# Performance work log

Hardware: AMD Instinct MI355X
Metric: run time of the kernel (lower is better)

## Reference

```python
import jax, jax.numpy as jnp
import numpy as np

N_NODES = 50000
N_EDGES = 500000
D_IN = 128
D_HID = 128
C = 1.0          # curvature (same for every layer)
MIN_NORM = 1e-15
MAX_TANH_ARG = 15.0
PROJ_EPS = 4e-3  # float32 boundary eps used by hgcn PoincareBall.proj


def _artanh(x):
    x = jnp.clip(x, -1.0 + 1e-7, 1.0 - 1e-7)
    return 0.5 * (jnp.log1p(x) - jnp.log1p(-x))


def _tanh(x):
    return jnp.tanh(jnp.clip(x, -MAX_TANH_ARG, MAX_TANH_ARG))


def _norm(x):
    return jnp.maximum(jnp.linalg.norm(x, axis=-1, keepdims=True), MIN_NORM)


def proj(x, c):
    # clip points to stay strictly inside the Poincare ball
    n = _norm(x)
    maxnorm = (1.0 - PROJ_EPS) / jnp.sqrt(c)
    return jnp.where(n > maxnorm, x / n * maxnorm, x)


def expmap0(u, c):
    sc = jnp.sqrt(c)
    n = _norm(u)
    return _tanh(sc * n) * u / (sc * n)


def logmap0(p, c):
    sc = jnp.sqrt(c)
    n = _norm(p)
    return _artanh(sc * n) * p / (sc * n)


def mobius_add(x, y, c):
    x2 = jnp.sum(x * x, -1, keepdims=True)
    y2 = jnp.sum(y * y, -1, keepdims=True)
    xy = jnp.sum(x * y, -1, keepdims=True)
    num = (1.0 + 2.0 * c * xy + c * y2) * x + (1.0 - c * x2) * y
    den = 1.0 + 2.0 * c * xy + c * c * x2 * y2
    return num / jnp.maximum(den, MIN_NORM)


def mobius_matvec(m, x, c):
    sc = jnp.sqrt(c)
    xn = _norm(x)
    mx = x @ m.T                                   # [N, out]
    mxn = _norm(mx)
    res = _tanh(mxn / xn * _artanh(sc * xn)) * mx / (mxn * sc)
    is_zero = jnp.all(mx == 0.0, axis=-1, keepdims=True)
    return jnp.where(is_zero, jnp.zeros_like(res), res)


def hyp_linear(x, W, b, c):
    h = proj(mobius_matvec(W, x, c), c)
    hyp_bias = proj(expmap0(b[None, :], c), c)     # proj_tan0 is identity on the ball
    return proj(mobius_add(h, hyp_bias, c), c)


def hyp_agg(x, src, dst, edge_weight, c):
    x_tan = logmap0(x, c)                          # [N, d] tangent at origin
    msg = edge_weight[:, None] * x_tan[src]        # [E, d] gather + scale
    agg = jax.ops.segment_sum(msg, dst, num_segments=N_NODES)  # spmm(adj, x_tan)
    return proj(expmap0(agg, c), c)


def hyp_act(x, c_in, c_out):
    xt = jax.nn.relu(logmap0(x, c_in))
    return proj(expmap0(xt, c_out), c_out)


def setup_inputs() -> dict:
    key = jax.random.key(0)
    ks = jax.random.split(key, 8)
    x = jax.random.normal(ks[0], (N_NODES, D_IN), dtype=jnp.float32) * 0.1
    src = jax.random.randint(ks[1], (N_EDGES,), 0, N_NODES)
    dst = jax.random.randint(ks[2], (N_EDGES,), 0, N_NODES)
    edge_weight = jax.random.uniform(ks[3], (N_EDGES,), dtype=jnp.float32) * 0.1
    s1 = 1.0 / np.sqrt(D_IN)
    W1 = jax.random.normal(ks[4], (D_HID, D_IN), dtype=jnp.float32) * s1
    b1 = jax.random.normal(ks[5], (D_HID,), dtype=jnp.float32) * 0.01
    W2 = jax.random.normal(ks[6], (D_HID, D_HID), dtype=jnp.float32) * s1
    b2 = jax.random.normal(ks[7], (D_HID,), dtype=jnp.float32) * 0.01
    return {"x": x, "src": src, "dst": dst, "edge_weight": edge_weight,
            "W1": W1, "b1": b1, "W2": W2, "b2": b2}


def reference(x, src, dst, edge_weight, W1, b1, W2, b2):
    c = jnp.float32(C)
    # HGCN.encode: proj_tan0 (identity for PoincareBall) -> expmap0 -> proj
    h = proj(expmap0(x, c), c)
    # layer 1: HypLinear -> HypAgg -> HypAct
    h = hyp_linear(h, W1, b1, c)
    h = hyp_agg(h, src, dst, edge_weight, c)
    h = hyp_act(h, c, c)
    # layer 2
    h = hyp_linear(h, W2, b2, c)
    h = hyp_agg(h, src, dst, edge_weight, c)
    h = hyp_act(h, c, c)
    return h
```

## Files before the change

### kernel.cpp

```cpp
#include <hip/hip_runtime.h>
#include <math.h>

#define MIN_NORM 1e-15f
#define MAXNORM  0.996f
#define ARTANH_CLIP 0.99999988f

typedef __bf16 bf16x8 __attribute__((ext_vector_type(8)));
typedef float  f32x4  __attribute__((ext_vector_type(4)));

union FragU { ushort u[8]; uint4 q; bf16x8 v; };

__device__ __forceinline__ float wave_sum(float v) {
#pragma unroll
    for (int off = 32; off > 0; off >>= 1) v += __shfl_xor(v, off, 64);
    return v;
}

__device__ __forceinline__ float tanh_fast(float x) {
    const float t = __expf(2.f * fminf(x, 15.f));
    return 1.f - 2.f / (t + 1.f);
}
__device__ __forceinline__ float artanh_fast(float x) {
    x = fminf(x, ARTANH_CLIP);
    return 0.5f * __logf((1.f + x) / (1.f - x));
}

__device__ __forceinline__ float proj_factor(float n2) {
    float n = fmaxf(sqrtf(n2), MIN_NORM);
    return (n > MAXNORM) ? (MAXNORM / n) : 1.f;
}

__device__ __forceinline__ unsigned short f2bf(float f) {
    unsigned u = __float_as_uint(f);
    return (unsigned short)((u + 0x7fffu + ((u >> 16) & 1u)) >> 16);
}
__device__ __forceinline__ float bf2f(unsigned short h) {
    return __uint_as_float((unsigned)h << 16);
}
__device__ __forceinline__ float bflo(unsigned u) { return __uint_as_float(u << 16); }
__device__ __forceinline__ float bfhi(unsigned u) { return __uint_as_float(u & 0xffff0000u); }

__device__ __forceinline__ void red16_f4(float4& v) {
#pragma unroll
    for (int off = 1; off < 16; off <<= 1) {
        v.x += __shfl_xor(v.x, off, 64);
        v.y += __shfl_xor(v.y, off, 64);
        v.z += __shfl_xor(v.z, off, 64);
        v.w += __shfl_xor(v.w, off, 64);
    }
}

__device__ __forceinline__ float bcast_row(const float4& v, int r) {
    const int src = (r >> 2) << 4;
    const float a = __shfl(v.x, src, 64);
    const float b = __shfl(v.y, src, 64);
    const float c = __shfl(v.z, src, 64);
    const float d = __shfl(v.w, src, 64);
    const float lo = (r & 1) ? b : a;
    const float hi = (r & 1) ? d : c;
    return (r & 2) ? hi : lo;
}

__device__ __forceinline__ void pack_w4(const float4 w4, int o, int k, char* out) {
    ushort4 h, l;
    h.x = f2bf(w4.x); l.x = f2bf(w4.x - bf2f(h.x));
    h.y = f2bf(w4.y); l.y = f2bf(w4.y - bf2f(h.y));
    h.z = f2bf(w4.z); l.z = f2bf(w4.z - bf2f(h.z));
    h.w = f2bf(w4.w); l.w = f2bf(w4.w - bf2f(h.w));
    const int prow = ((o & 7) << 4) | (o >> 3);
    const unsigned byte = (unsigned)((prow << 8) + (k << 1)) ^ (unsigned)((prow & 7) << 4);
    *reinterpret_cast<ushort4*>(out + byte) = h;
    *reinterpret_cast<ushort4*>(out + 32768 + byte) = l;
}

__global__ void zero_cnt(int* __restrict__ cnt, int N) {
    const int i = blockIdx.x * blockDim.x + threadIdx.x;
    if (i < N) cnt[i] = 0;
}

__global__ __launch_bounds__(256)
void setup_kernel(const float* __restrict__ W1, const float* __restrict__ W2,
                  char* __restrict__ g1, char* __restrict__ g2,
                  const float* __restrict__ b1, const float* __restrict__ b2,
                  float* __restrict__ hb1, float* __restrict__ hb2,
                  const int* __restrict__ dst, int* __restrict__ cnt, int E) {
    const int b = blockIdx.x;
    if (b < 32) {
        const float* W = (b < 16) ? W1 : W2;
        char* out = (b < 16) ? g1 : g2;
        const int i = (((b & 15) * 256) + threadIdx.x) * 4;
        pack_w4(*reinterpret_cast<const float4*>(&W[i]), i >> 7, i & 127, out);
    } else if (b == 32) {
        if (threadIdx.x < 64) {
            const int lane = threadIdx.x;
#pragma unroll
            for (int j = 0; j < 2; ++j) {
                const float* bb = j ? b2 : b1;
                float* hb = j ? hb2 : hb1;
                float v0 = bb[lane], v1 = bb[lane + 64];
                float n2 = wave_sum(v0 * v0 + v1 * v1);
                float n = fmaxf(sqrtf(n2), MIN_NORM);
                float sc = tanh_fast(n) / n;
                sc *= proj_factor(sc * sc * n2);
                hb[lane] = v0 * sc;
                hb[lane + 64] = v1 * sc;
            }
        }
    } else {
        const int e = (b - 33) * 256 + threadIdx.x;
        if (e < E) atomicAdd(&cnt[dst[e]], 1);
    }
}


__global__ void scan1(const int* __restrict__ cnt, int* __restrict__ ptr,
                      int* __restrict__ bsum, int N) {
    __shared__ int s[256];
    const int t = threadIdx.x;
    const int i = blockIdx.x * 256 + t;
    int v = (i < N) ? ((cnt[i] + 7) & ~7) : 0;
    s[t] = v;
    __syncthreads();
#pragma unroll
    for (int off = 1; off < 256; off <<= 1) {
        int add = (t >= off) ? s[t - off] : 0;
        __syncthreads();
        s[t] += add;
        __syncthreads();
    }
    if (i < N) ptr[i] = s[t] - v;
    if (t == 255) bsum[blockIdx.x] = s[255];
}

__global__ void scan2(const int* __restrict__ bsum, int* __restrict__ bscan, int nb) {
    __shared__ int s[256];
    const int t = threadIdx.x;
    int v = (t < nb) ? bsum[t] : 0;
    s[t] = v;
    __syncthreads();
#pragma unroll
    for (int off = 1; off < 256; off <<= 1) {
        int add = (t >= off) ? s[t - off] : 0;
        __syncthreads();
        s[t] += add;
        __syncthreads();
    }
    bscan[t] = s[t] - v;
    if (t == 255) bscan[256] = s[255];
}

__global__ void scan3(const int* __restrict__ bscan, const int* __restrict__ cnt,
                      int* __restrict__ ptr, int* __restrict__ cursor,
                      unsigned* __restrict__ epk, int N) {
    const int i = blockIdx.x * blockDim.x + threadIdx.x;
    if (i < N) {
        const int p = ptr[i] + bscan[i >> 8];
        ptr[i] = p;
        cursor[i] = p;
        const int c = cnt[i];
        const int pc = (c + 7) & ~7;
        for (int j = c; j < pc; ++j) epk[p + j] = 0u;
    }
    if (i == 0) {
        const int tot = bscan[256];
        ptr[N] = tot;
#pragma unroll
        for (int j = 0; j < 16; ++j) epk[tot + j] = 0u;
    }
}

__global__ void scatter_kernel(const int* __restrict__ src, const int* __restrict__ dst,
                               const float* __restrict__ ew, int* __restrict__ cursor,
                               unsigned* __restrict__ epk, int E) {
    int e = blockIdx.x * blockDim.x + threadIdx.x;
    if (e >= E) return;
    int pos = atomicAdd(&cursor[dst[e]], 1);
    epk[pos] = ((unsigned)src[e] << 16) | (unsigned)f2bf(ew[e]);
}

template <bool PRELUDE, bool BF16IN, bool BF16OUT>
__global__ __launch_bounds__(512, 4)
void hyp_linear_tan_mfma(const void* __restrict__ xin, const char* __restrict__ gWpack,
                         const float* __restrict__ hb, void* __restrict__ xtan,
                         int n_rows) {
    __shared__ __align__(16) char sW[65536];

    const int tid = threadIdx.x;
    const int lane = tid & 63, wid = tid >> 6;
    const int r15 = lane & 15, g = lane >> 4;

    const int tiles = (n_rows + 15) >> 4;
    const int tile = blockIdx.x * 8 + wid;
    const bool active = (tile < tiles);
    const int rowbase = tile << 4;
    const int myrow = rowbase + r15;
    const bool rok = active && (myrow < n_rows);

    float4 xa[4], xb[4];
    uint4 xu[4];
    if (BF16IN) {
        const char* xr = (const char*)xin + (size_t)myrow * 256 + g * 16;
#pragma unroll
        for (int kc = 0; kc < 4; ++kc)
            xu[kc] = rok ? *reinterpret_cast<const uint4*>(xr + kc * 64)
                         : make_uint4(0u, 0u, 0u, 0u);
    } else {
        const float* xr = (const float*)xin + (size_t)myrow * 128 + g * 8;
#pragma unroll
        for (int kc = 0; kc < 4; ++kc) {
            if (rok) {
                xa[kc] = *reinterpret_cast<const float4*>(xr + kc * 32);
                xb[kc] = *reinterpret_cast<const float4*>(xr + kc * 32 + 4);
            } else {
                xa[kc] = make_float4(0.f, 0.f, 0.f, 0.f);
                xb[kc] = xa[kc];
            }
        }
    }

    {
        const uint4* gsrc = reinterpret_cast<const uint4*>(gWpack);
        uint4* ldst = reinterpret_cast<uint4*>(sW);
#pragma unroll
        for (int i = 0; i < 8; ++i) ldst[tid + i * 512] = gsrc[tid + i * 512];
    }

    float yb[8];
    {
        const float4 yba = *reinterpret_cast<const float4*>(&hb[r15 * 8]);
        const float4 ybb = *reinterpret_cast<const float4*>(&hb[r15 * 8 + 4]);
        yb[0] = yba.x; yb[1] = yba.y; yb[2] = yba.z; yb[3] = yba.w;
        yb[4] = ybb.x; yb[5] = ybb.y; yb[6] = ybb.z; yb[7] = ybb.w;
    }
    float y2p = 0.f;
#pragma unroll
    for (int t = 0; t < 8; ++t) y2p += yb[t] * yb[t];
#pragma unroll
    for (int off = 1; off < 16; off <<= 1) y2p += __shfl_xor(y2p, off, 64);
    const float y2 = y2p;

    __syncthreads();
    if (!active) return;

    bf16x8 ah[4], al[4];
    float ss = 0.f;
    if (BF16IN) {
#pragma unroll
        for (int kc = 0; kc < 4; ++kc) {
            FragU fu; fu.q = xu[kc];
            ah[kc] = fu.v;
            const uint4 u = xu[kc];
            float f0 = bflo(u.x), f1 = bfhi(u.x), f2_ = bflo(u.y), f3 = bfhi(u.y);
            float f4 = bflo(u.z), f5 = bfhi(u.z), f6 = bflo(u.w), f7 = bfhi(u.w);
            ss += f0 * f0 + f1 * f1 + f2_ * f2_ + f3 * f3
                + f4 * f4 + f5 * f5 + f6 * f6 + f7 * f7;
        }
    } else {
#pragma unroll
        for (int kc = 0; kc < 4; ++kc) {
            const float4 a = xa[kc], b = xb[kc];
            ss += a.x * a.x + a.y * a.y + a.z * a.z + a.w * a.w
                + b.x * b.x + b.y * b.y + b.z * b.z + b.w * b.w;
            ah[kc][0] = (__bf16)a.x; al[kc][0] = (__bf16)(a.x - (float)ah[kc][0]);
            ah[kc][1] = (__bf16)a.y; al[kc][1] = (__bf16)(a.y - (float)ah[kc][1]);
            ah[kc][2] = (__bf16)a.z; al[kc][2] = (__bf16)(a.z - (float)ah[kc][2]);
            ah[kc][3] = (__bf16)a.w; al[kc][3] = (__bf16)(a.w - (float)ah[kc][3]);
            ah[kc][4] = (__bf16)b.x; al[kc][4] = (__bf16)(b.x - (float)ah[kc][4]);
            ah[kc][5] = (__bf16)b.y; al[kc][5] = (__bf16)(b.y - (float)ah[kc][5]);
            ah[kc][6] = (__bf16)b.z; al[kc][6] = (__bf16)(b.z - (float)ah[kc][6]);
            ah[kc][7] = (__bf16)b.w; al[kc][7] = (__bf16)(b.w - (float)ah[kc][7]);
        }
    }
    ss += __shfl_xor(ss, 16, 64);
    ss += __shfl_xor(ss, 32, 64);

    f32x4 acc[8];
#pragma unroll
    for (int ct = 0; ct < 8; ++ct) acc[ct] = (f32x4){0.f, 0.f, 0.f, 0.f};

    const unsigned lswz = (unsigned)((r15 & 7) << 4);
#pragma unroll
    for (int kc = 0; kc < 4; ++kc) {
#pragma unroll
        for (int ct = 0; ct < 8; ++ct) {
            const unsigned byte =
                ((unsigned)((ct << 12) + (r15 << 8) + (kc << 6) + (g << 4))) ^ lswz;
            FragU bh, bl;
            bh.q = *reinterpret_cast<const uint4*>(sW + byte);
            bl.q = *reinterpret_cast<const uint4*>(sW + 32768 + byte);
            acc[ct] = __builtin_amdgcn_mfma_f32_16x16x32_bf16(ah[kc], bh.v, acc[ct], 0, 0, 0);
            acc[ct] = __builtin_amdgcn_mfma_f32_16x16x32_bf16(ah[kc], bl.v, acc[ct], 0, 0, 0);
            if (!BF16IN)
                acc[ct] = __builtin_amdgcn_mfma_f32_16x16x32_bf16(al[kc], bh.v, acc[ct], 0, 0, 0);
        }
    }

    float4 r2 = make_float4(0.f, 0.f, 0.f, 0.f);
    float4 xyv = make_float4(0.f, 0.f, 0.f, 0.f);
#pragma unroll
    for (int ct = 0; ct < 8; ++ct) {
        r2.x += acc[ct][0] * acc[ct][0];
        r2.y += acc[ct][1] * acc[ct][1];
        r2.z += acc[ct][2] * acc[ct][2];
        r2.w += acc[ct][3] * acc[ct][3];
        xyv.x += acc[ct][0] * yb[ct];
        xyv.y += acc[ct][1] * yb[ct];
        xyv.z += acc[ct][2] * yb[ct];
        xyv.w += acc[ct][3] * yb[ct];
    }
    red16_f4(r2);
    red16_f4(xyv);

    const float rn2 = bcast_row(r2, r15);
    const float xyr = bcast_row(xyv, r15);
    const float n2v = ss;

    const float n = fmaxf(sqrtf(n2v), MIN_NORM);
    float sc = 1.f;
    if (PRELUDE) {
        sc = tanh_fast(n) / n;
        sc *= proj_factor(sc * sc * n2v);
    }
    const float xn = fmaxf(sc * n, MIN_NORM);
    const float mxn = fmaxf(sc * sqrtf(rn2), MIN_NORM);
    const float s = tanh_fast(mxn / xn * artanh_fast(xn));
    const float sl0 = (s * sc) / mxn;
    float m2 = rn2 * sl0 * sl0;
    const float f = proj_factor(m2);
    const float scl = sl0 * f;
    m2 *= f * f;
    const float xy = scl * xyr;
    const float cx = 1.f + 2.f * xy + y2;
    const float cy = 1.f - m2;
    const float rdn = 1.f / fmaxf(1.f + 2.f * xy + m2 * y2, MIN_NORM);
    const float A = cx * scl * rdn;
    const float B = cy * rdn;
    const float on2 = A * A * rn2 + 2.f * A * B * xyr + B * B * y2;
    const float f2 = proj_factor(on2);
    const float onn = fmaxf(sqrtf(on2) * f2, MIN_NORM);
    const float slg = artanh_fast(onn) / onn;
    const float P = slg * f2 * A;
    const float Q = slg * f2 * B;

#pragma unroll
    for (int reg = 0; reg < 4; ++reg) {
        const float Pr = __shfl(P, 4 * g + reg, 64);
        const float Qr = __shfl(Q, 4 * g + reg, 64);
        const int row = rowbase + 4 * g + reg;
        if (row < n_rows) {
            float v[8];
#pragma unroll
            for (int ct = 0; ct < 8; ++ct)
                v[ct] = fmaf(Pr, acc[ct][reg], Qr * yb[ct]);
            if (BF16OUT) {
                uint4 pk;
                pk.x = (unsigned)f2bf(v[0]) | ((unsigned)f2bf(v[1]) << 16);
                pk.y = (unsigned)f2bf(v[2]) | ((unsigned)f2bf(v[3]) << 16);
                pk.z = (unsigned)f2bf(v[4]) | ((unsigned)f2bf(v[5]) << 16);
                pk.w = (unsigned)f2bf(v[6]) | ((unsigned)f2bf(v[7]) << 16);
                *reinterpret_cast<uint4*>((char*)xtan + (size_t)row * 256 + r15 * 16) = pk;
            } else {
                float* orow = (float*)xtan + (size_t)row * 128 + r15 * 8;
                *reinterpret_cast<float4*>(orow) = make_float4(v[0], v[1], v[2], v[3]);
                *reinterpret_cast<float4*>(orow + 4) = make_float4(v[4], v[5], v[6], v[7]);
            }
        }
    }
}

template <bool BF16OUT>
__global__ __launch_bounds__(1024)
void gather_act(const char* __restrict__ xt, const int* __restrict__ ptr,
                const unsigned* __restrict__ epk, void* __restrict__ out, int n_rows) {
    const int v = blockIdx.x * 16 + (threadIdx.x >> 6);
    if (v >= n_rows) return;
    const int lane = threadIdx.x & 63;
    const int q = lane >> 4, t = lane & 15;
    const char* xtl = xt + (t << 4);
    const int beg = ptr[v];
    const int it = (ptr[v + 1] - beg) >> 3;

    float acc[8], bcc[8];
#pragma unroll
    for (int j = 0; j < 8; ++j) { acc[j] = 0.f; bcc[j] = 0.f; }

    const unsigned* ep = epk + beg + q;
    unsigned p0 = 0u, p1 = 0u;
    if (it > 0) { p0 = ep[0]; p1 = ep[4]; }
    for (int k = 1; k <= it; ++k) {
        const uint4 u0 = *reinterpret_cast<const uint4*>(xtl + ((p0 >> 16) << 8));
        const uint4 u1 = *reinterpret_cast<const uint4*>(xtl + ((p1 >> 16) << 8));
        const unsigned n0 = ep[k * 8];
        const unsigned n1 = ep[k * 8 + 4];
        const float w0 = __uint_as_float(p0 << 16);
        const float w1 = __uint_as_float(p1 << 16);
        acc[0] = fmaf(w0, bflo(u0.x), acc[0]);  bcc[0] = fmaf(w1, bflo(u1.x), bcc[0]);
        acc[1] = fmaf(w0, bfhi(u0.x), acc[1]);  bcc[1] = fmaf(w1, bfhi(u1.x), bcc[1]);
        acc[2] = fmaf(w0, bflo(u0.y), acc[2]);  bcc[2] = fmaf(w1, bflo(u1.y), bcc[2]);
        acc[3] = fmaf(w0, bfhi(u0.y), acc[3]);  bcc[3] = fmaf(w1, bfhi(u1.y), bcc[3]);
        acc[4] = fmaf(w0, bflo(u0.z), acc[4]);  bcc[4] = fmaf(w1, bflo(u1.z), bcc[4]);
        acc[5] = fmaf(w0, bfhi(u0.z), acc[5]);  bcc[5] = fmaf(w1, bfhi(u1.z), bcc[5]);
        acc[6] = fmaf(w0, bflo(u0.w), acc[6]);  bcc[6] = fmaf(w1, bflo(u1.w), bcc[6]);
        acc[7] = fmaf(w0, bfhi(u0.w), acc[7]);  bcc[7] = fmaf(w1, bfhi(u1.w), bcc[7]);
        p0 = n0; p1 = n1;
    }
#pragma unroll
    for (int j = 0; j < 8; ++j) acc[j] += bcc[j];

#pragma unroll
    for (int j = 0; j < 8; ++j) {
        acc[j] += __shfl_xor(acc[j], 16, 64);
        acc[j] += __shfl_xor(acc[j], 32, 64);
    }

    float s = 0.f;
#pragma unroll
    for (int j = 0; j < 8; ++j) s += acc[j] * acc[j];
#pragma unroll
    for (int off = 1; off < 16; off <<= 1) s += __shfl_xor(s, off, 64);
    const float n2 = s;

    float n = fmaxf(sqrtf(n2), MIN_NORM);
    float sc = tanh_fast(n) / n;
    float hn2 = sc * sc * n2;
    float f = proj_factor(hn2);
    sc *= f; hn2 *= f * f;
    float hn = fmaxf(sqrtf(hn2), MIN_NORM);
    float sl = artanh_fast(hn) / hn;
    const float scl1 = sc * sl;

    float x[8];
    float s2 = 0.f;
#pragma unroll
    for (int j = 0; j < 8; ++j) {
        x[j] = fmaxf(acc[j] * scl1, 0.f);
        s2 += x[j] * x[j];
    }
#pragma unroll
    for (int off = 1; off < 16; off <<= 1) s2 += __shfl_xor(s2, off, 64);
    float nb = fmaxf(sqrtf(s2), MIN_NORM);
    float scb = tanh_fast(nb) / nb;
    scb *= proj_factor(scb * scb * s2);

    const float o0 = x[2 * q] * scb, o1 = x[2 * q + 1] * scb;
    if (BF16OUT) {
        const unsigned pk = (unsigned)f2bf(o0) | ((unsigned)f2bf(o1) << 16);
        *reinterpret_cast<unsigned*>((char*)out + (size_t)v * 256 + t * 16 + q * 4) = pk;
    } else {
        *reinterpret_cast<float2*>((float*)out + (size_t)v * 128 + t * 8 + q * 2) =
            make_float2(o0, o1);
    }
}

__global__ __launch_bounds__(256)
void agg_edges(const float* __restrict__ xtan, const int* __restrict__ src,
               const int* __restrict__ dst, const float* __restrict__ ew,
               float* __restrict__ agg, int n_edges) {
    int gt = blockIdx.x * blockDim.x + threadIdx.x;
    int e = gt >> 5;
    if (e >= n_edges) return;
    int c = (gt & 31) << 2;
    int sN = src[e], dN = dst[e];
    float w = ew[e];
    const float4 v = *reinterpret_cast<const float4*>(&xtan[(size_t)sN * 128 + c]);
    float* ap = &agg[(size_t)dN * 128 + c];
    atomicAdd(ap + 0, w * v.x);
    atomicAdd(ap + 1, w * v.y);
    atomicAdd(ap + 2, w * v.z);
    atomicAdd(ap + 3, w * v.w);
}

__global__ __launch_bounds__(256)
void hyp_act_kernel(const float* __restrict__ in, float* __restrict__ out, int n_rows) {
    int row = blockIdx.x * 4 + (threadIdx.x >> 6);
    if (row >= n_rows) return;
    int lane = threadIdx.x & 63;
    int l2 = lane << 1;
    const float2 v = *reinterpret_cast<const float2*>(&in[(size_t)row * 128 + l2]);
    float a0 = v.x, a1 = v.y;
    float n2 = wave_sum(a0 * a0 + a1 * a1);
    float n = fmaxf(sqrtf(n2), MIN_NORM);
    float sc = tanh_fast(n) / n;
    float hn2 = sc * sc * n2;
    float f = proj_factor(hn2);
    sc *= f; hn2 *= f * f;
    float h0 = a0 * sc, h1 = a1 * sc;
    float hn = fmaxf(sqrtf(hn2), MIN_NORM);
    float sl = artanh_fast(hn) / hn;
    float x0 = fmaxf(h0 * sl, 0.f), x1 = fmaxf(h1 * sl, 0.f);
    float n2b = wave_sum(x0 * x0 + x1 * x1);
    float nb = fmaxf(sqrtf(n2b), MIN_NORM);
    float scb = tanh_fast(nb) / nb;
    scb *= proj_factor(scb * scb * n2b);
    *reinterpret_cast<float2*>(&out[(size_t)row * 128 + l2]) =
        make_float2(x0 * scb, x1 * scb);
}

__global__ void bias_kernel(const float* __restrict__ b1, const float* __restrict__ b2,
                            float* __restrict__ hb1, float* __restrict__ hb2) {
    int lane = threadIdx.x;
#pragma unroll
    for (int j = 0; j < 2; ++j) {
        const float* b = j ? b2 : b1;
        float* hb = j ? hb2 : hb1;
        float v0 = b[lane], v1 = b[lane + 64];
        float n2 = wave_sum(v0 * v0 + v1 * v1);
        float n = fmaxf(sqrtf(n2), MIN_NORM);
        float sc = tanh_fast(n) / n;
        sc *= proj_factor(sc * sc * n2);
        hb[lane] = v0 * sc;
        hb[lane + 64] = v1 * sc;
    }
}

__global__ void prep_w(const float* __restrict__ W1, const float* __restrict__ W2,
                       char* __restrict__ g1, char* __restrict__ g2) {
    const int b = blockIdx.x;
    const float* W = (b < 16) ? W1 : W2;
    char* out = (b < 16) ? g1 : g2;
    const int i = (((b & 15) * 256) + threadIdx.x) * 4;
    pack_w4(*reinterpret_cast<const float4*>(&W[i]), i >> 7, i & 127, out);
}

extern "C" void kernel_launch(void* const* d_in, const int* in_sizes, int n_in,
                              void* d_out, int out_size, void* d_ws, size_t ws_size,
                              hipStream_t stream) {
    const float* x   = (const float*)d_in[0];
    const int*   src = (const int*)d_in[1];
    const int*   dst = (const int*)d_in[2];
    const float* ew  = (const float*)d_in[3];
    const float* W1  = (const float*)d_in[4];
    const float* b1  = (const float*)d_in[5];
    const float* W2  = (const float*)d_in[6];
    const float* b2  = (const float*)d_in[7];

    const int N = in_sizes[0] / 128;
    const int E = in_sizes[1];
    float* fout = (float*)d_out;

    const int tiles = (N + 15) >> 4;
    const int lin_grid = (tiles + 7) / 8;
    const int nbE = (E + 255) / 256;
    const int nbN = (N + 255) / 256;
    const int gat_grid = (N + 15) / 16;

    const size_t epk_words = (size_t)E + 7 * (size_t)N + 16;

    const size_t need = 131072 + 1024
                      + (size_t)N * 256 * 2
                      + (epk_words + N) * 4
                      + ((size_t)(N + 1) + N) * 4
                      + 4096;

    if (ws_size >= need) {
        char*  base  = (char*)d_ws;
        char*  gW1p  = base;
        char*  gW2p  = base + 65536;
        float* hb1   = (float*)(base + 131072);
        float* hb2   = hb1 + 128;
        char*  xtA   = base + 131072 + 1024;
        char*  xtB   = xtA + (size_t)N * 256;
        unsigned* epk = (unsigned*)(xtB + (size_t)N * 256);
        int* cnt     = (int*)(epk + epk_words);
        int* ptr     = cnt + N;
        int* cursor  = ptr + (N + 1);
        int* bsum    = cursor + N;
        int* bscan   = bsum + 256;

        zero_cnt<<<nbN, 256, 0, stream>>>(cnt, N);
        setup_kernel<<<33 + nbE, 256, 0, stream>>>(W1, W2, gW1p, gW2p,
                                                   b1, b2, hb1, hb2, dst, cnt, E);
        scan1<<<nbN, 256, 0, stream>>>(cnt, ptr, bsum, N);
        scan2<<<1, 256, 0, stream>>>(bsum, bscan, nbN);
        scan3<<<nbN, 256, 0, stream>>>(bscan, cnt, ptr, cursor, epk, N);
        scatter_kernel<<<nbE, 256, 0, stream>>>(src, dst, ew, cursor, epk, E);

        hyp_linear_tan_mfma<true, false, true><<<lin_grid, 512, 0, stream>>>(x, gW1p, hb1, xtA, N);
        gather_act<true><<<gat_grid, 1024, 0, stream>>>(xtA, ptr, epk, xtB, N);
        hyp_linear_tan_mfma<false, true, true><<<lin_grid, 512, 0, stream>>>(xtB, gW2p, hb2, xtA, N);
        gather_act<false><<<gat_grid, 1024, 0, stream>>>(xtA, ptr, epk, fout, N);
    } else {
        char*  gW1p = (char*)d_ws;
        char*  gW2p = gW1p + 65536;
        float* hb1  = (float*)(gW2p + 65536);
        float* hb2  = hb1 + 128;
        float* nbuf = hb2 + 128;
        const size_t node_bytes = (size_t)N * 128 * sizeof(float);
        const int agg_blocks = (int)(((size_t)E * 32 + 255) / 256);
        const int row_blocks = (N + 3) / 4;

        prep_w<<<32, 256, 0, stream>>>(W1, W2, gW1p, gW2p);
        bias_kernel<<<1, 64, 0, stream>>>(b1, b2, hb1, hb2);
        hyp_linear_tan_mfma<true, false, false><<<lin_grid, 512, 0, stream>>>(x, gW1p, hb1, fout, N);
        hipMemsetAsync(nbuf, 0, node_bytes, stream);
        agg_edges<<<agg_blocks, 256, 0, stream>>>(fout, src, dst, ew, nbuf, E);
        hyp_act_kernel<<<row_blocks, 256, 0, stream>>>(nbuf, nbuf, N);
        hyp_linear_tan_mfma<false, false, false><<<lin_grid, 512, 0, stream>>>(nbuf, gW2p, hb2, fout, N);
        hipMemsetAsync(fout, 0, node_bytes, stream);
        agg_edges<<<agg_blocks, 256, 0, stream>>>(fout, src, dst, ew, nbuf, E);
        hyp_act_kernel<<<row_blocks, 256, 0, stream>>>(nbuf, fout, N);
    }
}
```

Baseline: 174.5 us.

## Fuse edge scatter into first linear kernel and pad linear grid to 512 blocks

```diff
diff --git a/kernel.cpp b/kernel.cpp
--- a/kernel.cpp
+++ b/kernel.cpp
@@ -169,28 +169,17 @@
     }
 }
 
-__global__ void scatter_kernel(const int* __restrict__ src, const int* __restrict__ dst,
-                               const float* __restrict__ ew, int* __restrict__ cursor,
-                               unsigned* __restrict__ epk, int E) {
-    int e = blockIdx.x * blockDim.x + threadIdx.x;
-    if (e >= E) return;
-    int pos = atomicAdd(&cursor[dst[e]], 1);
-    epk[pos] = ((unsigned)src[e] << 16) | (unsigned)f2bf(ew[e]);
-}
-
 template <bool PRELUDE, bool BF16IN, bool BF16OUT>
-__global__ __launch_bounds__(512, 4)
-void hyp_linear_tan_mfma(const void* __restrict__ xin, const char* __restrict__ gWpack,
-                         const float* __restrict__ hb, void* __restrict__ xtan,
-                         int n_rows) {
-    __shared__ __align__(16) char sW[65536];
-
+__device__ __forceinline__
+void linear_body(char* sW, int bid, int ngrid,
+                 const void* __restrict__ xin, const char* __restrict__ gWpack,
+                 const float* __restrict__ hb, void* __restrict__ xtan, int n_rows) {
     const int tid = threadIdx.x;
     const int lane = tid & 63, wid = tid >> 6;
     const int r15 = lane & 15, g = lane >> 4;
 
     const int tiles = (n_rows + 15) >> 4;
-    const int tile = blockIdx.x * 8 + wid;
+    const int tile = bid + ngrid * wid;
     const bool active = (tile < tiles);
     const int rowbase = tile << 4;
     const int myrow = rowbase + r15;
@@ -366,6 +355,43 @@
             }
         }
     }
+}
+
+template <bool PRELUDE, bool BF16IN, bool BF16OUT>
+__global__ __launch_bounds__(512, 4)
+void hyp_linear_tan_mfma(const void* __restrict__ xin, const char* __restrict__ gWpack,
+                         const float* __restrict__ hb, void* __restrict__ xtan,
+                         int n_rows, int ngrid) {
+    __shared__ __align__(16) char sW[65536];
+    linear_body<PRELUDE, BF16IN, BF16OUT>(sW, blockIdx.x, ngrid, xin, gWpack, hb, xtan, n_rows);
+}
+
+__global__ __launch_bounds__(512, 4)
+void linear1_scatter(const void* __restrict__ xin, const char* __restrict__ gWpack,
+                     const float* __restrict__ hb, void* __restrict__ xtan, int n_rows,
+                     int ngrid,
+                     const int* __restrict__ src, const int* __restrict__ dst,
+                     const float* __restrict__ ew, int* __restrict__ cursor,
+                     unsigned* __restrict__ epk, int E) {
+    __shared__ __align__(16) char sW[65536];
+    if ((int)blockIdx.x < ngrid) {
+        linear_body<true, false, true>(sW, blockIdx.x, ngrid, xin, gWpack, hb, xtan, n_rows);
+    } else {
+        const int e = ((int)blockIdx.x - ngrid) * 512 + (int)threadIdx.x;
+        if (e < E) {
+            const int pos = atomicAdd(&cursor[dst[e]], 1);
+            epk[pos] = ((unsigned)src[e] << 16) | (unsigned)f2bf(ew[e]);
+        }
+    }
+}
+
+__global__ void scatter_kernel(const int* __restrict__ src, const int* __restrict__ dst,
+                               const float* __restrict__ ew, int* __restrict__ cursor,
+                               unsigned* __restrict__ epk, int E) {
+    int e = blockIdx.x * blockDim.x + threadIdx.x;
+    if (e >= E) return;
+    int pos = atomicAdd(&cursor[dst[e]], 1);
+    epk[pos] = ((unsigned)src[e] << 16) | (unsigned)f2bf(ew[e]);
 }
 
 template <bool BF16OUT>
@@ -539,9 +565,11 @@
     float* fout = (float*)d_out;
 
     const int tiles = (N + 15) >> 4;
-    const int lin_grid = (tiles + 7) / 8;
+    int lin_grid = (tiles + 7) / 8;
+    if (lin_grid < 512) lin_grid = 512;
     const int nbE = (E + 255) / 256;
     const int nbN = (N + 255) / 256;
+    const int nbS = (E + 511) / 512;
     const int gat_grid = (N + 15) / 16;
 
     const size_t epk_words = (size_t)E + 7 * (size_t)N + 16;
@@ -573,11 +601,12 @@
         scan1<<<nbN, 256, 0, stream>>>(cnt, ptr, bsum, N);
         scan2<<<1, 256, 0, stream>>>(bsum, bscan, nbN);
         scan3<<<nbN, 256, 0, stream>>>(bscan, cnt, ptr, cursor, epk, N);
-        scatter_kernel<<<nbE, 256, 0, stream>>>(src, dst, ew, cursor, epk, E);
-
-        hyp_linear_tan_mfma<true, false, true><<<lin_grid, 512, 0, stream>>>(x, gW1p, hb1, xtA, N);
+
+        linear1_scatter<<<lin_grid + nbS, 512, 0, stream>>>(
+            x, gW1p, hb1, xtA, N, lin_grid, src, dst, ew, cursor, epk, E);
         gather_act<true><<<gat_grid, 1024, 0, stream>>>(xtA, ptr, epk, xtB, N);
-        hyp_linear_tan_mfma<false, true, true><<<lin_grid, 512, 0, stream>>>(xtB, gW2p, hb2, xtA, N);
+        hyp_linear_tan_mfma<false, true, true><<<lin_grid, 512, 0, stream>>>(
+            xtB, gW2p, hb2, xtA, N, lin_grid);
         gather_act<false><<<gat_grid, 1024, 0, stream>>>(xtA, ptr, epk, fout, N);
     } else {
         char*  gW1p = (char*)d_ws;
@@ -591,11 +620,13 @@
 
         prep_w<<<32, 256, 0, stream>>>(W1, W2, gW1p, gW2p);
         bias_kernel<<<1, 64, 0, stream>>>(b1, b2, hb1, hb2);
-        hyp_linear_tan_mfma<true, false, false><<<lin_grid, 512, 0, stream>>>(x, gW1p, hb1, fout, N);
+        hyp_linear_tan_mfma<true, false, false><<<lin_grid, 512, 0, stream>>>(
+            x, gW1p, hb1, fout, N, lin_grid);
         hipMemsetAsync(nbuf, 0, node_bytes, stream);
         agg_edges<<<agg_blocks, 256, 0, stream>>>(fout, src, dst, ew, nbuf, E);
         hyp_act_kernel<<<row_blocks, 256, 0, stream>>>(nbuf, nbuf, N);
-        hyp_linear_tan_mfma<false, false, false><<<lin_grid, 512, 0, stream>>>(nbuf, gW2p, hb2, fout, N);
+        hyp_linear_tan_mfma<false, false, false><<<lin_grid, 512, 0, stream>>>(
+            nbuf, gW2p, hb2, fout, N, lin_grid);
         hipMemsetAsync(fout, 0, node_bytes, stream);
         agg_edges<<<agg_blocks, 256, 0, stream>>>(fout, src, dst, ew, nbuf, E);
         hyp_act_kernel<<<row_blocks, 256, 0, stream>>>(nbuf, fout, N);
```

Measured after the change: 170.3 us. -2.4%, faster.
